# Optimization experiments

Hardware: AMD Instinct MI355X
Metric: run time of the kernel (lower is better)

The kernel has to match this reference:

```python
import jax, jax.numpy as jnp
import numpy as np

B, S, HID, NH = 4, 1024, 1024, 16
HD = HID // NH  # 64


def setup_inputs() -> dict:
    key = jax.random.key(0)
    ks = jax.random.split(key, 8)
    scale = 0.02
    return {
        "attention_mask": jnp.zeros((B, 1, 1, S), dtype=jnp.float32),
        "query": jax.random.normal(ks[0], (B, S, HID), dtype=jnp.float32),
        "key": jax.random.normal(ks[1], (B, S, HID), dtype=jnp.float32),
        "value": jax.random.normal(ks[2], (B, S, HID), dtype=jnp.float32),
        "Wq": jax.random.normal(ks[3], (HID, HID), dtype=jnp.float32) * scale,
        "bq": jnp.zeros((HID,), dtype=jnp.float32),
        "Wk": jax.random.normal(ks[4], (HID, HID), dtype=jnp.float32) * scale,
        "bk": jnp.zeros((HID,), dtype=jnp.float32),
    }


def reference(attention_mask, query, key, value, Wq, bq, Wk, bk):
    # Linear projections (torch Linear: x @ W.T + b)
    q = query @ Wq.T + bq  # [B,S,HID]
    k = key @ Wk.T + bk    # [B,S,HID]
    # split heads -> [B,NH,S,HD]
    q = q.reshape(B, S, NH, HD).transpose(0, 2, 1, 3)
    k = k.reshape(B, S, NH, HD).transpose(0, 2, 1, 3)
    scores = jnp.einsum("bhqd,bhkd->bhqk", q, k) / jnp.sqrt(jnp.float32(HD))
    scores = scores + attention_mask  # additive mask broadcast [B,1,1,S]
    probs = jax.nn.softmax(scores, axis=-1)  # [B,NH,S,S]
    # V is shared across heads; head-mean folds into a single contraction:
    # mean_h(probs_h @ V) = (sum_h probs_h) @ V / NH
    out = jnp.einsum("bhqk,bkv->bqv", probs, value) / NH  # [B,S,HID]
    return out
```

## Files before the change

kernel.cpp:

```cpp
#include <hip/hip_runtime.h>
#include <hip/hip_fp16.h>

#define B_    4
#define S_    1024
#define HID_  1024
#define NH_   16
#define HD_   64

#define LOG2E 1.44269504f

typedef _Float16 half8 __attribute__((ext_vector_type(8)));
typedef float f32x4 __attribute__((ext_vector_type(4)));

__device__ __forceinline__ half8 cvt8(float4 a, float4 b) {
    half8 h;
    h[0] = (_Float16)a.x; h[1] = (_Float16)a.y;
    h[2] = (_Float16)a.z; h[3] = (_Float16)a.w;
    h[4] = (_Float16)b.x; h[5] = (_Float16)b.y;
    h[6] = (_Float16)b.z; h[7] = (_Float16)b.w;
    return h;
}

__device__ __forceinline__ float fexp2(float x) {
#if __has_builtin(__builtin_amdgcn_exp2f)
    return __builtin_amdgcn_exp2f(x);
#else
    float r;
    asm("v_exp_f32 %0, %1\n\ts_nop 0" : "=v"(r) : "v"(x));
    return r;
#endif
}

__device__ __forceinline__ void gll16(const _Float16* g, _Float16* l) {
    __builtin_amdgcn_global_load_lds(
        (const __attribute__((address_space(1))) unsigned int*)g,
        (__attribute__((address_space(3))) unsigned int*)l, 16, 0, 0);
}

__global__ __launch_bounds__(256) void cast_f16(
    const float* __restrict__ query, const float* __restrict__ key,
    const float* __restrict__ Wq, const float* __restrict__ Wk,
    const float* __restrict__ V,
    _Float16* __restrict__ Af16, _Float16* __restrict__ Wf16,
    _Float16* __restrict__ Vt)
{
    __shared__ float t[32][33];
    const int x = blockIdx.x;
    if (blockIdx.y == 0) {
        long base = ((long)x * 256 + threadIdx.x) * 8;
        const float* src = (x < 2048) ? (query + base) : (key + base - (4l << 20));
        float4 v0 = *(const float4*)src, v1 = *(const float4*)(src + 4);
        *(half8*)(Af16 + base) = cvt8(v0, v1);
    } else if (blockIdx.y == 1) {
        if (x >= 1024) return;
        long base = ((long)x * 256 + threadIdx.x) * 8;
        const float* src = (x < 512) ? (Wq + base) : (Wk + base - (1l << 20));
        float4 v0 = *(const float4*)src, v1 = *(const float4*)(src + 4);
        *(half8*)(Wf16 + base) = cvt8(v0, v1);
    } else {
        const int b  = x >> 10;
        const int s0 = ((x >> 5) & 31) * 32;
        const int h0 = (x & 31) * 32;
        const int tx = threadIdx.x & 31, ty = threadIdx.x >> 5;
#pragma unroll
        for (int rr = 0; rr < 4; rr++) {
            int s = s0 + ty + rr * 8;
            t[ty + rr * 8][tx] = V[((long)b * S_ + s) * HID_ + h0 + tx];
        }
        __syncthreads();
#pragma unroll
        for (int rr = 0; rr < 4; rr++) {
            int h = h0 + ty + rr * 8;
            Vt[((long)b * HID_ + h) * S_ + s0 + tx] = (_Float16)t[tx][ty + rr * 8];
        }
    }
}

__global__ __launch_bounds__(256) void proj_qk_f16(
    const _Float16* __restrict__ Af16,
    const _Float16* __restrict__ Wf16,
    const float* __restrict__ bq, const float* __restrict__ bk,
    _Float16* __restrict__ Oq, _Float16* __restrict__ Ok)
{
    const int f  = blockIdx.x + 16 * blockIdx.y + 512 * blockIdx.z;
    const int w2 = (f & 7) * 128 + (f >> 3);
    const int bx = w2 & 15, by = (w2 >> 4) & 31, bz = w2 >> 9;

    const _Float16* A    = Af16 + (long)bz * 4096 * 1024;
    const _Float16* Wm   = Wf16 + (long)bz * 1024 * 1024;
    const float*    bias = bz ? bk : bq;
    _Float16*       Co   = bz ? Ok : Oq;

    __shared__ _Float16 Al[2][128 * 32];
    __shared__ _Float16 Bl[2][64 * 32];

    const int tid  = threadIdx.x;
    const int wv   = tid >> 6;
    const int lane = tid & 63;
    const int l15  = lane & 15;
    const int quad = lane >> 4;
    const int wm   = wv & 1, wn = wv >> 1;
    const int m0   = by * 128, n0 = bx * 64;

    const int srA  = (lane >> 2);
    const int scA  = (lane & 3) * 8;
    const _Float16* gA0 = A  + (long)(m0 + wv * 16 + srA) * 1024 + scA;
    const _Float16* gA1 = A  + (long)(m0 + 64 + wv * 16 + srA) * 1024 + scA;
    const _Float16* gB  = Wm + (long)(n0 + wv * 16 + srA) * 1024 + scA;
    const int ldsW = wv * 512;

    f32x4 acc[4][2];
#pragma unroll
    for (int i = 0; i < 4; i++)
#pragma unroll
        for (int j = 0; j < 2; j++) acc[i][j] = (f32x4){0.f, 0.f, 0.f, 0.f};

    gll16(gA0, &Al[0][ldsW]);
    gll16(gA1, &Al[0][2048 + ldsW]);
    gll16(gB,  &Bl[0][ldsW]);
    __syncthreads();

#pragma unroll 2
    for (int kt = 0; kt < HID_; kt += 32) {
        const int p = (kt >> 5) & 1;

        if (kt + 32 < HID_) {
            gll16(gA0 + kt + 32, &Al[p ^ 1][ldsW]);
            gll16(gA1 + kt + 32, &Al[p ^ 1][2048 + ldsW]);
            gll16(gB  + kt + 32, &Bl[p ^ 1][ldsW]);
        }

        half8 af[4], bf[2];
#pragma unroll
        for (int i = 0; i < 4; i++)
            af[i] = *(const half8*)(&Al[p][(wm * 64 + i * 16 + l15) * 32 + quad * 8]);
#pragma unroll
        for (int j = 0; j < 2; j++)
            bf[j] = *(const half8*)(&Bl[p][(wn * 32 + j * 16 + l15) * 32 + quad * 8]);

#pragma unroll
        for (int i = 0; i < 4; i++)
#pragma unroll
            for (int j = 0; j < 2; j++)
                acc[i][j] = __builtin_amdgcn_mfma_f32_16x16x32_f16(
                    af[i], bf[j], acc[i][j], 0, 0, 0);

        __syncthreads();
    }

    const int isQ = (bz == 0);
#pragma unroll
    for (int j = 0; j < 2; j++) {
        int col = n0 + wn * 32 + j * 16 + l15;
        float bv = bias[col];
        int h = col >> 6, d = col & 63, pp = d >> 3, jj = d & 7;
#pragma unroll
        for (int i = 0; i < 4; i++) {
            int row = m0 + wm * 64 + i * 16 + quad * 4;
            int bb = row >> 10, ss = row & 1023;
            long base;
            if (isQ)
                base = ((((long)(bb * NH_ + h) * 64 + (ss >> 4)) * 8 + pp) * 16
                        + (ss & 15)) * 8 + jj;
            else
                base = (((long)(bb * NH_ + h) * 8 + pp) * 1024 + ss) * 8 + jj;
#pragma unroll
            for (int r = 0; r < 4; r++)
                Co[base + r * 8] = (_Float16)(acc[i][j][r] + bv);
        }
    }
}

__global__ __launch_bounds__(512) void attn_psum_f16(
    const _Float16* __restrict__ qb,
    const _Float16* __restrict__ kb,
    const float* __restrict__ mask,
    _Float16* __restrict__ psum)
{
    const int f   = blockIdx.x + 64 * blockIdx.y;
    const int w2s = (f & 7) * 32 + (f >> 3);
    const int qt  = w2s & 63;
    const int b   = w2s >> 6;

    const int q0   = qt * 16;
    const int tid  = threadIdx.x;
    const int w    = tid >> 6;
    const int lane = tid & 63;
    const int l15  = lane & 15;
    const int quad = lane >> 4;

    __shared__ float redS[2][16][8];

    const float SC = 0.125f * LOG2E;

    float mreg[8];
#pragma unroll
    for (int t = 0; t < 8; t++)
        mreg[t] = mask[b * S_ + t * 128 + w * 16 + l15] * LOG2E;

    f32x4 acc[8];
#pragma unroll
    for (int t = 0; t < 8; t++) acc[t] = (f32x4){0.f, 0.f, 0.f, 0.f};

    for (int h = 0; h < NH_; h++) {
        const _Float16* qh = qb + ((long)(b * NH_ + h) * 64 + qt) * 1024;
        const _Float16* kh = kb + (long)(b * NH_ + h) * 8192 * 8;

        half8 a0 = *(const half8*)(qh + quad * 128 + l15 * 8);
        half8 a1 = *(const half8*)(qh + (quad + 4) * 128 + l15 * 8);

        f32x4 s[8];
#pragma unroll
        for (int cc = 0; cc < 8; cc++) {
            const int key = cc * 128 + w * 16 + l15;
            half8 b0 = *(const half8*)(kh + (long)quad * 8192 + key * 8);
            half8 b1 = *(const half8*)(kh + (long)(quad + 4) * 8192 + key * 8);
            f32x4 c = (f32x4){0.f, 0.f, 0.f, 0.f};
            c = __builtin_amdgcn_mfma_f32_16x16x32_f16(a0, b0, c, 0, 0, 0);
            c = __builtin_amdgcn_mfma_f32_16x16x32_f16(a1, b1, c, 0, 0, 0);
            s[cc] = c;
        }

        const int p = h & 1;
        float sm[4] = {0.f, 0.f, 0.f, 0.f};
#pragma unroll
        for (int t = 0; t < 8; t++)
#pragma unroll
            for (int r = 0; r < 4; r++) {
                float pr = fexp2(fmaf(s[t][r], SC, mreg[t]));
                s[t][r] = pr;
                sm[r] += pr;
            }
#pragma unroll
        for (int off = 1; off < 16; off <<= 1)
#pragma unroll
            for (int r = 0; r < 4; r++) sm[r] += __shfl_xor(sm[r], off);
        if (l15 == 0)
#pragma unroll
            for (int r = 0; r < 4; r++) redS[p][quad * 4 + r][w] = sm[r];
        __syncthreads();

#pragma unroll
        for (int r = 0; r < 4; r++) {
            float4 v0 = *(float4*)&redS[p][quad * 4 + r][0];
            float4 v1 = *(float4*)&redS[p][quad * 4 + r][4];
            float tot = (v0.x + v0.y + v0.z + v0.w) + (v1.x + v1.y + v1.z + v1.w);
            float inv = 1.f / tot;
#pragma unroll
            for (int t = 0; t < 8; t++) acc[t][r] += s[t][r] * inv;
        }
    }

    _Float16* prow = psum + (long)(b * S_ + q0) * S_;
#pragma unroll
    for (int t = 0; t < 8; t++)
#pragma unroll
        for (int r = 0; r < 4; r++) {
            int row = quad * 4 + r;
            prow[(long)row * S_ + t * 128 + w * 16 + l15] = (_Float16)acc[t][r];
        }
}

__global__ __launch_bounds__(256) void pv_f16(
    const _Float16* __restrict__ Pc,
    const _Float16* __restrict__ Vt,
    float* __restrict__ out)
{
    const int f   = blockIdx.x + 16 * blockIdx.y + 128 * blockIdx.z;
    const int xcd = f & 7, ii = f >> 3;
    const int bx  = ii & 15;
    const int by  = (ii >> 4) + ((xcd & 1) << 2);
    const int b   = xcd >> 1;

    const _Float16* A  = Pc + (long)b * S_ * S_;
    const _Float16* Bm = Vt + (long)b * HID_ * S_;

    __shared__ _Float16 Al[2][128 * 32];
    __shared__ _Float16 Bl[2][64 * 32];

    const int tid  = threadIdx.x;
    const int wv   = tid >> 6;
    const int lane = tid & 63;
    const int l15  = lane & 15;
    const int quad = lane >> 4;
    const int wm   = wv & 1, wn = wv >> 1;
    const int m0   = by * 128, n0 = bx * 64;

    const int srA  = (lane >> 2);
    const int scA  = (lane & 3) * 8;
    const _Float16* gA0 = A  + (long)(m0 + wv * 16 + srA) * S_ + scA;
    const _Float16* gA1 = A  + (long)(m0 + 64 + wv * 16 + srA) * S_ + scA;
    const _Float16* gB  = Bm + (long)(n0 + wv * 16 + srA) * S_ + scA;
    const int ldsW = wv * 512;

    f32x4 acc[4][2];
#pragma unroll
    for (int i = 0; i < 4; i++)
#pragma unroll
        for (int j = 0; j < 2; j++) acc[i][j] = (f32x4){0.f, 0.f, 0.f, 0.f};

    gll16(gA0, &Al[0][ldsW]);
    gll16(gA1, &Al[0][2048 + ldsW]);
    gll16(gB,  &Bl[0][ldsW]);
    __syncthreads();

#pragma unroll 2
    for (int kt = 0; kt < S_; kt += 32) {
        const int p = (kt >> 5) & 1;

        if (kt + 32 < S_) {
            gll16(gA0 + kt + 32, &Al[p ^ 1][ldsW]);
            gll16(gA1 + kt + 32, &Al[p ^ 1][2048 + ldsW]);
            gll16(gB  + kt + 32, &Bl[p ^ 1][ldsW]);
        }

        half8 af[4], bf[2];
#pragma unroll
        for (int i = 0; i < 4; i++)
            af[i] = *(const half8*)(&Al[p][(wm * 64 + i * 16 + l15) * 32 + quad * 8]);
#pragma unroll
        for (int j = 0; j < 2; j++)
            bf[j] = *(const half8*)(&Bl[p][(wn * 32 + j * 16 + l15) * 32 + quad * 8]);

#pragma unroll
        for (int i = 0; i < 4; i++)
#pragma unroll
            for (int j = 0; j < 2; j++)
                acc[i][j] = __builtin_amdgcn_mfma_f32_16x16x32_f16(
                    af[i], bf[j], acc[i][j], 0, 0, 0);

        __syncthreads();
    }

    const float alpha = 1.f / NH_;
#pragma unroll
    for (int i = 0; i < 4; i++) {
        int row = m0 + wm * 64 + i * 16 + quad * 4;
#pragma unroll
        for (int j = 0; j < 2; j++) {
            int col = n0 + wn * 32 + j * 16 + l15;
#pragma unroll
            for (int r = 0; r < 4; r++)
                out[(long)(b * S_ + row + r) * HID_ + col] = acc[i][j][r] * alpha;
        }
    }
}

extern "C" void kernel_launch(void* const* d_in, const int* in_sizes, int n_in,
                              void* d_out, int out_size, void* d_ws, size_t ws_size,
                              hipStream_t stream)
{
    const float* mask  = (const float*)d_in[0];
    const float* query = (const float*)d_in[1];
    const float* key   = (const float*)d_in[2];
    const float* value = (const float*)d_in[3];
    const float* Wq    = (const float*)d_in[4];
    const float* bq    = (const float*)d_in[5];
    const float* Wk    = (const float*)d_in[6];
    const float* bk    = (const float*)d_in[7];
    float* out = (float*)d_out;

    char* ws = (char*)d_ws;
    const long MB = 1l << 20;
    _Float16* qbuf = (_Float16*)(ws);
    _Float16* kbuf = (_Float16*)(ws + 8 * MB);
    _Float16* Af16 = (_Float16*)(ws + 16 * MB);
    _Float16* Wf16 = (_Float16*)(ws + 32 * MB);
    _Float16* Vt   = (_Float16*)(ws + 36 * MB);
    _Float16* psum = (_Float16*)(ws + 16 * MB);

    cast_f16<<<dim3(4096, 3), dim3(256), 0, stream>>>(
        query, key, Wq, Wk, value, Af16, Wf16, Vt);

    proj_qk_f16<<<dim3(16, 32, 2), dim3(256), 0, stream>>>(
        Af16, Wf16, bq, bk, qbuf, kbuf);

    attn_psum_f16<<<dim3(64, B_), dim3(512), 0, stream>>>(
        qbuf, kbuf, mask, psum);

    pv_f16<<<dim3(16, 8, B_), dim3(256), 0, stream>>>(psum, Vt, out);
}
```

Before: 202.6 us.

## Split head loop across two blocks and sum partial probs inside PV loader

The attention-probability kernel now splits the 16 heads into two halves on a third grid dimension, doubling the block count from 256 to 512 for better CU occupancy. Each half writes its own partial probability sum to a separate buffer. The PV GEMM reads both buffers through registers, adds them in fp16 while staging into padded LDS (stride 40) to cut bank conflicts, and uses a register-prefetch double buffer in place of global_load_lds. Q fragments for the next head are prefetched. In exchange the PV kernel reads twice the P traffic, and summing the two halves in fp16 adds a little rounding.

```diff
diff --git a/kernel.cpp b/kernel.cpp
--- a/kernel.cpp
+++ b/kernel.cpp
@@ -8,6 +8,7 @@
 #define HD_   64
 
 #define LOG2E 1.44269504f
+#define PSTR  40
 
 typedef _Float16 half8 __attribute__((ext_vector_type(8)));
 typedef float f32x4 __attribute__((ext_vector_type(4)));
@@ -29,6 +30,12 @@
     asm("v_exp_f32 %0, %1\n\ts_nop 0" : "=v"(r) : "v"(x));
     return r;
 #endif
+}
+
+__device__ __forceinline__ void lds_barrier() {
+    asm volatile("s_waitcnt lgkmcnt(0)" ::: "memory");
+    __builtin_amdgcn_s_barrier();
+    __builtin_amdgcn_sched_barrier(0);
 }
 
 __device__ __forceinline__ void gll16(const _Float16* g, _Float16* l) {
@@ -177,10 +184,11 @@
     const float* __restrict__ mask,
     _Float16* __restrict__ psum)
 {
-    const int f   = blockIdx.x + 64 * blockIdx.y;
-    const int w2s = (f & 7) * 32 + (f >> 3);
+    const int f   = blockIdx.x + 64 * blockIdx.y + 256 * blockIdx.z;
+    const int w2s = (f & 7) * 64 + (f >> 3);
     const int qt  = w2s & 63;
-    const int b   = w2s >> 6;
+    const int b   = (w2s >> 6) & 3;
+    const int hz  = w2s >> 8;
 
     const int q0   = qt * 16;
     const int tid  = threadIdx.x;
@@ -202,12 +210,14 @@
 #pragma unroll
     for (int t = 0; t < 8; t++) acc[t] = (f32x4){0.f, 0.f, 0.f, 0.f};
 
-    for (int h = 0; h < NH_; h++) {
-        const _Float16* qh = qb + ((long)(b * NH_ + h) * 64 + qt) * 1024;
+    const int h0 = hz * 8;
+    const _Float16* qh0 = qb + ((long)(b * NH_ + h0) * 64 + qt) * 1024;
+    half8 a0 = *(const half8*)(qh0 + quad * 128 + l15 * 8);
+    half8 a1 = *(const half8*)(qh0 + (quad + 4) * 128 + l15 * 8);
+
+    for (int i = 0; i < 8; i++) {
+        const int h = h0 + i;
         const _Float16* kh = kb + (long)(b * NH_ + h) * 8192 * 8;
-
-        half8 a0 = *(const half8*)(qh + quad * 128 + l15 * 8);
-        half8 a1 = *(const half8*)(qh + (quad + 4) * 128 + l15 * 8);
 
         f32x4 s[8];
 #pragma unroll
@@ -221,7 +231,13 @@
             s[cc] = c;
         }
 
-        const int p = h & 1;
+        if (i < 7) {
+            const _Float16* qh = qb + ((long)(b * NH_ + h + 1) * 64 + qt) * 1024;
+            a0 = *(const half8*)(qh + quad * 128 + l15 * 8);
+            a1 = *(const half8*)(qh + (quad + 4) * 128 + l15 * 8);
+        }
+
+        const int p = i & 1;
         float sm[4] = {0.f, 0.f, 0.f, 0.f};
 #pragma unroll
         for (int t = 0; t < 8; t++)
@@ -251,7 +267,7 @@
         }
     }
 
-    _Float16* prow = psum + (long)(b * S_ + q0) * S_;
+    _Float16* prow = psum + (long)hz * ((long)B_ * S_ * S_) + (long)(b * S_ + q0) * S_;
 #pragma unroll
     for (int t = 0; t < 8; t++)
 #pragma unroll
@@ -272,11 +288,13 @@
     const int by  = (ii >> 4) + ((xcd & 1) << 2);
     const int b   = xcd >> 1;
 
-    const _Float16* A  = Pc + (long)b * S_ * S_;
+    const long QS = (long)B_ * S_ * S_;
+    const _Float16* A0 = Pc + (long)b * S_ * S_;
+    const _Float16* A1 = A0 + QS;
     const _Float16* Bm = Vt + (long)b * HID_ * S_;
 
-    __shared__ _Float16 Al[2][128 * 32];
-    __shared__ _Float16 Bl[2][64 * 32];
+    __shared__ _Float16 Al[2][128 * PSTR];
+    __shared__ _Float16 Bl[2][64 * PSTR];
 
     const int tid  = threadIdx.x;
     const int wv   = tid >> 6;
@@ -285,13 +303,14 @@
     const int quad = lane >> 4;
     const int wm   = wv & 1, wn = wv >> 1;
     const int m0   = by * 128, n0 = bx * 64;
-
-    const int srA  = (lane >> 2);
-    const int scA  = (lane & 3) * 8;
-    const _Float16* gA0 = A  + (long)(m0 + wv * 16 + srA) * S_ + scA;
-    const _Float16* gA1 = A  + (long)(m0 + 64 + wv * 16 + srA) * S_ + scA;
-    const _Float16* gB  = Bm + (long)(n0 + wv * 16 + srA) * S_ + scA;
-    const int ldsW = wv * 512;
+    const int sr   = tid >> 2;
+    const int sc   = (tid & 3) * 8;
+
+    const _Float16* a00 = A0 + (long)(m0 + sr) * S_ + sc;
+    const _Float16* a01 = A1 + (long)(m0 + sr) * S_ + sc;
+    const _Float16* a10 = A0 + (long)(m0 + 64 + sr) * S_ + sc;
+    const _Float16* a11 = A1 + (long)(m0 + 64 + sr) * S_ + sc;
+    const _Float16* bp0 = Bm + (long)(n0 + sr) * S_ + sc;
 
     f32x4 acc[4][2];
 #pragma unroll
@@ -299,37 +318,50 @@
 #pragma unroll
         for (int j = 0; j < 2; j++) acc[i][j] = (f32x4){0.f, 0.f, 0.f, 0.f};
 
-    gll16(gA0, &Al[0][ldsW]);
-    gll16(gA1, &Al[0][2048 + ldsW]);
-    gll16(gB,  &Bl[0][ldsW]);
-    __syncthreads();
+    half8 c00 = *(const half8*)(a00), c01 = *(const half8*)(a01);
+    half8 c10 = *(const half8*)(a10), c11 = *(const half8*)(a11);
+    half8 cb  = *(const half8*)(bp0);
+    *(half8*)&Al[0][sr * PSTR + sc]        = c00 + c01;
+    *(half8*)&Al[0][(64 + sr) * PSTR + sc] = c10 + c11;
+    *(half8*)&Bl[0][sr * PSTR + sc]        = cb;
+    c00 = *(const half8*)(a00 + 32); c01 = *(const half8*)(a01 + 32);
+    c10 = *(const half8*)(a10 + 32); c11 = *(const half8*)(a11 + 32);
+    cb  = *(const half8*)(bp0 + 32);
+    lds_barrier();
 
 #pragma unroll 2
     for (int kt = 0; kt < S_; kt += 32) {
         const int p = (kt >> 5) & 1;
 
+        half8 af[4], bfm[2];
+#pragma unroll
+        for (int i = 0; i < 4; i++)
+            af[i] = *(const half8*)(&Al[p][(wm * 64 + i * 16 + l15) * PSTR + quad * 8]);
+#pragma unroll
+        for (int j = 0; j < 2; j++)
+            bfm[j] = *(const half8*)(&Bl[p][(wn * 32 + j * 16 + l15) * PSTR + quad * 8]);
+
         if (kt + 32 < S_) {
-            gll16(gA0 + kt + 32, &Al[p ^ 1][ldsW]);
-            gll16(gA1 + kt + 32, &Al[p ^ 1][2048 + ldsW]);
-            gll16(gB  + kt + 32, &Bl[p ^ 1][ldsW]);
-        }
-
-        half8 af[4], bf[2];
-#pragma unroll
-        for (int i = 0; i < 4; i++)
-            af[i] = *(const half8*)(&Al[p][(wm * 64 + i * 16 + l15) * 32 + quad * 8]);
-#pragma unroll
-        for (int j = 0; j < 2; j++)
-            bf[j] = *(const half8*)(&Bl[p][(wn * 32 + j * 16 + l15) * 32 + quad * 8]);
+            *(half8*)&Al[p ^ 1][sr * PSTR + sc]        = c00 + c01;
+            *(half8*)&Al[p ^ 1][(64 + sr) * PSTR + sc] = c10 + c11;
+            *(half8*)&Bl[p ^ 1][sr * PSTR + sc]        = cb;
+            if (kt + 64 < S_) {
+                c00 = *(const half8*)(a00 + kt + 64);
+                c01 = *(const half8*)(a01 + kt + 64);
+                c10 = *(const half8*)(a10 + kt + 64);
+                c11 = *(const half8*)(a11 + kt + 64);
+                cb  = *(const half8*)(bp0 + kt + 64);
+            }
+        }
 
 #pragma unroll
         for (int i = 0; i < 4; i++)
 #pragma unroll
             for (int j = 0; j < 2; j++)
                 acc[i][j] = __builtin_amdgcn_mfma_f32_16x16x32_f16(
-                    af[i], bf[j], acc[i][j], 0, 0, 0);
-
-        __syncthreads();
+                    af[i], bfm[j], acc[i][j], 0, 0, 0);
+
+        lds_barrier();
     }
 
     const float alpha = 1.f / NH_;
@@ -367,7 +399,7 @@
     _Float16* Af16 = (_Float16*)(ws + 16 * MB);
     _Float16* Wf16 = (_Float16*)(ws + 32 * MB);
     _Float16* Vt   = (_Float16*)(ws + 36 * MB);
-    _Float16* psum = (_Float16*)(ws + 16 * MB);
+    _Float16* Ph   = (_Float16*)(ws + 16 * MB);
 
     cast_f16<<<dim3(4096, 3), dim3(256), 0, stream>>>(
         query, key, Wq, Wk, value, Af16, Wf16, Vt);
@@ -375,8 +407,8 @@
     proj_qk_f16<<<dim3(16, 32, 2), dim3(256), 0, stream>>>(
         Af16, Wf16, bq, bk, qbuf, kbuf);
 
-    attn_psum_f16<<<dim3(64, B_), dim3(512), 0, stream>>>(
-        qbuf, kbuf, mask, psum);
-
-    pv_f16<<<dim3(16, 8, B_), dim3(256), 0, stream>>>(psum, Vt, out);
-}
+    attn_psum_f16<<<dim3(64, B_, 2), dim3(512), 0, stream>>>(
+        qbuf, kbuf, mask, Ph);
+
+    pv_f16<<<dim3(16, 8, B_), dim3(256), 0, stream>>>(Ph, Vt, out);
+}
```

Measured after the change: 200.2 us. Within noise of the previous version (-1.2%).

## Split attention head loop across four blocks and combine partial prob sums

Applied to the files above, without the earlier changes.

The attention-probability kernel previously launched only 256 blocks, each looping over all 16 heads. It now splits the heads into 4 groups on a third grid dimension, giving 1024 blocks, and writes 4 partial fp16 probability sums. A new kernel adds these partials together and also performs the V transpose, which moves out of the cast kernel. The Q fragment for the next head is prefetched during the current head's work. In exchange, the change adds 32MB of partial-sum writes and reads plus one extra launch, and reuses workspace regions.

```diff
diff --git a/kernel.cpp b/kernel.cpp
--- a/kernel.cpp
+++ b/kernel.cpp
@@ -40,39 +40,20 @@
 __global__ __launch_bounds__(256) void cast_f16(
     const float* __restrict__ query, const float* __restrict__ key,
     const float* __restrict__ Wq, const float* __restrict__ Wk,
-    const float* __restrict__ V,
-    _Float16* __restrict__ Af16, _Float16* __restrict__ Wf16,
-    _Float16* __restrict__ Vt)
-{
-    __shared__ float t[32][33];
+    _Float16* __restrict__ Af16, _Float16* __restrict__ Wf16)
+{
     const int x = blockIdx.x;
     if (blockIdx.y == 0) {
         long base = ((long)x * 256 + threadIdx.x) * 8;
         const float* src = (x < 2048) ? (query + base) : (key + base - (4l << 20));
         float4 v0 = *(const float4*)src, v1 = *(const float4*)(src + 4);
         *(half8*)(Af16 + base) = cvt8(v0, v1);
-    } else if (blockIdx.y == 1) {
+    } else {
         if (x >= 1024) return;
         long base = ((long)x * 256 + threadIdx.x) * 8;
         const float* src = (x < 512) ? (Wq + base) : (Wk + base - (1l << 20));
         float4 v0 = *(const float4*)src, v1 = *(const float4*)(src + 4);
         *(half8*)(Wf16 + base) = cvt8(v0, v1);
-    } else {
-        const int b  = x >> 10;
-        const int s0 = ((x >> 5) & 31) * 32;
-        const int h0 = (x & 31) * 32;
-        const int tx = threadIdx.x & 31, ty = threadIdx.x >> 5;
-#pragma unroll
-        for (int rr = 0; rr < 4; rr++) {
-            int s = s0 + ty + rr * 8;
-            t[ty + rr * 8][tx] = V[((long)b * S_ + s) * HID_ + h0 + tx];
-        }
-        __syncthreads();
-#pragma unroll
-        for (int rr = 0; rr < 4; rr++) {
-            int h = h0 + ty + rr * 8;
-            Vt[((long)b * HID_ + h) * S_ + s0 + tx] = (_Float16)t[tx][ty + rr * 8];
-        }
     }
 }
 
@@ -175,12 +156,13 @@
     const _Float16* __restrict__ qb,
     const _Float16* __restrict__ kb,
     const float* __restrict__ mask,
-    _Float16* __restrict__ psum)
-{
-    const int f   = blockIdx.x + 64 * blockIdx.y;
-    const int w2s = (f & 7) * 32 + (f >> 3);
+    _Float16* __restrict__ P)
+{
+    const int f   = blockIdx.x + 64 * blockIdx.y + 256 * blockIdx.z;
+    const int w2s = (f & 7) * 128 + (f >> 3);
     const int qt  = w2s & 63;
-    const int b   = w2s >> 6;
+    const int b   = (w2s >> 6) & 3;
+    const int hz  = w2s >> 8;
 
     const int q0   = qt * 16;
     const int tid  = threadIdx.x;
@@ -202,12 +184,14 @@
 #pragma unroll
     for (int t = 0; t < 8; t++) acc[t] = (f32x4){0.f, 0.f, 0.f, 0.f};
 
-    for (int h = 0; h < NH_; h++) {
-        const _Float16* qh = qb + ((long)(b * NH_ + h) * 64 + qt) * 1024;
+    const int hb = hz * 4;
+    const _Float16* qh0 = qb + ((long)(b * NH_ + hb) * 64 + qt) * 1024;
+    half8 a0 = *(const half8*)(qh0 + quad * 128 + l15 * 8);
+    half8 a1 = *(const half8*)(qh0 + (quad + 4) * 128 + l15 * 8);
+
+    for (int ii = 0; ii < 4; ii++) {
+        const int h = hb + ii;
         const _Float16* kh = kb + (long)(b * NH_ + h) * 8192 * 8;
-
-        half8 a0 = *(const half8*)(qh + quad * 128 + l15 * 8);
-        half8 a1 = *(const half8*)(qh + (quad + 4) * 128 + l15 * 8);
 
         f32x4 s[8];
 #pragma unroll
@@ -221,7 +205,13 @@
             s[cc] = c;
         }
 
-        const int p = h & 1;
+        if (ii < 3) {
+            const _Float16* qh = qb + ((long)(b * NH_ + h + 1) * 64 + qt) * 1024;
+            a0 = *(const half8*)(qh + quad * 128 + l15 * 8);
+            a1 = *(const half8*)(qh + (quad + 4) * 128 + l15 * 8);
+        }
+
+        const int p = ii & 1;
         float sm[4] = {0.f, 0.f, 0.f, 0.f};
 #pragma unroll
         for (int t = 0; t < 8; t++)
@@ -251,7 +241,7 @@
         }
     }
 
-    _Float16* prow = psum + (long)(b * S_ + q0) * S_;
+    _Float16* prow = P + (long)hz * ((long)B_ * S_ * S_) + (long)(b * S_ + q0) * S_;
 #pragma unroll
     for (int t = 0; t < 8; t++)
 #pragma unroll
@@ -259,6 +249,44 @@
             int row = quad * 4 + r;
             prow[(long)row * S_ + t * 128 + w * 16 + l15] = (_Float16)acc[t][r];
         }
+}
+
+__global__ __launch_bounds__(256) void vt_combine(
+    const _Float16* __restrict__ P, _Float16* __restrict__ o,
+    const float* __restrict__ V, _Float16* __restrict__ Vt)
+{
+    __shared__ float t[32][33];
+    if (blockIdx.y == 0) {
+        if (blockIdx.x >= 2048) return;
+        const long QS = (long)B_ * S_ * S_;
+        long i = (long)(blockIdx.x * 256 + threadIdx.x) * 8;
+        half8 a = *(const half8*)(P + i);
+        half8 b = *(const half8*)(P + QS + i);
+        half8 c = *(const half8*)(P + 2 * QS + i);
+        half8 d = *(const half8*)(P + 3 * QS + i);
+        half8 r;
+#pragma unroll
+        for (int e = 0; e < 8; e++)
+            r[e] = (_Float16)((float)a[e] + (float)b[e] + (float)c[e] + (float)d[e]);
+        *(half8*)(o + i) = r;
+    } else {
+        const int x  = blockIdx.x;
+        const int b  = x >> 10;
+        const int s0 = ((x >> 5) & 31) * 32;
+        const int h0 = (x & 31) * 32;
+        const int tx = threadIdx.x & 31, ty = threadIdx.x >> 5;
+#pragma unroll
+        for (int rr = 0; rr < 4; rr++) {
+            int s = s0 + ty + rr * 8;
+            t[ty + rr * 8][tx] = V[((long)b * S_ + s) * HID_ + h0 + tx];
+        }
+        __syncthreads();
+#pragma unroll
+        for (int rr = 0; rr < 4; rr++) {
+            int h = h0 + ty + rr * 8;
+            Vt[((long)b * HID_ + h) * S_ + s0 + tx] = (_Float16)t[tx][ty + rr * 8];
+        }
+    }
 }
 
 __global__ __launch_bounds__(256) void pv_f16(
@@ -366,17 +394,20 @@
     _Float16* kbuf = (_Float16*)(ws + 8 * MB);
     _Float16* Af16 = (_Float16*)(ws + 16 * MB);
     _Float16* Wf16 = (_Float16*)(ws + 32 * MB);
-    _Float16* Vt   = (_Float16*)(ws + 36 * MB);
-    _Float16* psum = (_Float16*)(ws + 16 * MB);
-
-    cast_f16<<<dim3(4096, 3), dim3(256), 0, stream>>>(
-        query, key, Wq, Wk, value, Af16, Wf16, Vt);
+    _Float16* Pq   = (_Float16*)(ws + 16 * MB);
+    _Float16* Vt   = (_Float16*)(ws);
+    _Float16* psum = (_Float16*)(ws + 8 * MB);
+
+    cast_f16<<<dim3(4096, 2), dim3(256), 0, stream>>>(
+        query, key, Wq, Wk, Af16, Wf16);
 
     proj_qk_f16<<<dim3(16, 32, 2), dim3(256), 0, stream>>>(
         Af16, Wf16, bq, bk, qbuf, kbuf);
 
-    attn_psum_f16<<<dim3(64, B_), dim3(512), 0, stream>>>(
-        qbuf, kbuf, mask, psum);
+    attn_psum_f16<<<dim3(S_ / 16, B_, 4), dim3(512), 0, stream>>>(
+        qbuf, kbuf, mask, Pq);
+
+    vt_combine<<<dim3(4096, 2), dim3(256), 0, stream>>>(Pq, psum, value, Vt);
 
     pv_f16<<<dim3(16, 8, B_), dim3(256), 0, stream>>>(psum, Vt, out);
 }
```

Measured after the change: 207.7 us. 2.5% more time.
